# Kernel optimization log

Measured on AMD Instinct MI355X. Metric: run time of the kernel, lower is better.

The kernel has to match this reference:

```python
import jax, jax.numpy as jnp
import numpy as np

B, C, D, H, W = 2, 96, 40, 96, 96
K = 256
OUT = (7, 7, 7)        # (PD, PH, PW)
SCALE = 0.25           # x/y spatial scale
SCALE_D = 0.5          # z (depth) spatial scale
SR = 2                 # sampling_ratio


def setup_inputs() -> dict:
    key = jax.random.key(0)
    k1, k2, k3, k4 = jax.random.split(key, 4)
    x = jax.random.normal(k1, (B, C, D, H, W), dtype=jnp.float32)
    # ROIs in original-image coordinates: x/y in [0, W/SCALE), z in [0, D/SCALE_D)
    img_w, img_h, img_d = W / SCALE, H / SCALE, D / SCALE_D
    bidx = jax.random.randint(k2, (K, 1), 0, B).astype(jnp.float32)
    starts = jax.random.uniform(k3, (K, 3)) * jnp.array([img_w * 0.7, img_h * 0.7, img_d * 0.7])
    sizes = 8.0 + jax.random.uniform(k4, (K, 3)) * jnp.array([img_w * 0.3, img_h * 0.3, img_d * 0.3])
    ends = starts + sizes
    rois = jnp.concatenate([bidx, starts, ends], axis=1).astype(jnp.float32)  # [K,7]
    return {"input_tensor": x, "rois": rois}


def _lin(coord, size):
    # Trilinear 1D component: indices low/high + weights, zeroed outside [-1, size].
    valid = (coord >= -1.0) & (coord <= size)
    c = jnp.clip(coord, 0.0, size - 1)
    low = jnp.floor(c).astype(jnp.int32)
    high = jnp.minimum(low + 1, size - 1)
    frac = c - low.astype(c.dtype)
    wl = jnp.where(valid, 1.0 - frac, 0.0)
    wh = jnp.where(valid, frac, 0.0)
    return low, high, wl, wh


def _sample_coords(start, length, pooled, sr):
    # start, length: [K] -> sample coords [K, pooled*sr]
    bin_sz = length / pooled
    p = jnp.arange(pooled, dtype=start.dtype)
    s = (jnp.arange(sr, dtype=start.dtype) + 0.5) / sr
    c = start[:, None, None] + (p[None, :, None] + s[None, None, :]) * bin_sz[:, None, None]
    return c.reshape(start.shape[0], pooled * sr)


def reference(input_tensor, rois):
    PD, PH, PW = OUT
    bidx = rois[:, 0].astype(jnp.int32)
    x1 = rois[:, 1] * SCALE; y1 = rois[:, 2] * SCALE; z1 = rois[:, 3] * SCALE_D
    x2 = rois[:, 4] * SCALE; y2 = rois[:, 5] * SCALE; z2 = rois[:, 6] * SCALE_D
    rw = jnp.maximum(x2 - x1, 1.0)
    rh = jnp.maximum(y2 - y1, 1.0)
    rd = jnp.maximum(z2 - z1, 1.0)
    cz = _sample_coords(z1, rd, PD, SR)  # [K, PD*SR]
    cy = _sample_coords(y1, rh, PH, SR)  # [K, PH*SR]
    cx = _sample_coords(x1, rw, PW, SR)  # [K, PW*SR]
    zl, zh, wzl, wzh = _lin(cz, D)
    yl, yh, wyl, wyh = _lin(cy, H)
    xl, xh, wxl, wxh = _lin(cx, W)
    b = bidx[:, None, None, None]

    def gather(zi, yi, xi):
        # advanced indexing -> [K, Zs, Ys, Xs, C]
        return input_tensor[b, :, zi[:, :, None, None], yi[:, None, :, None], xi[:, None, None, :]]

    out = jnp.zeros((K, PD * SR, PH * SR, PW * SR, C), dtype=input_tensor.dtype)
    for zi, wz in ((zl, wzl), (zh, wzh)):
        for yi, wy in ((yl, wyl), (yh, wyh)):
            for xi, wx in ((xl, wxl), (xh, wxh)):
                w = wz[:, :, None, None] * wy[:, None, :, None] * wx[:, None, None, :]
                out = out + gather(zi, yi, xi) * w[..., None]
    # average the SR^3 samples inside each output bin
    out = out.reshape(K, PD, SR, PH, SR, PW, SR, C).mean(axis=(2, 4, 6))
    return out.transpose(0, 4, 1, 2, 3)  # [K, C, PD, PH, PW]
```

## Files before the change

### kernel.cpp

```cpp
#include <hip/hip_runtime.h>
#include <hip/hip_fp16.h>


#define Bn 2
#define Cn 96
#define Dn 40
#define Hn 96
#define Wn 96
#define Kn 256
#define CELLS 343
#define NS 14
#define MAXZ 18
#define MAXY 32
#define MAXROWS (MAXZ * MAXY)
#define SLOTS 18
#define DHWc (Dn * Hn * Wn)

typedef float float2u __attribute__((ext_vector_type(2), aligned(4)));

__global__ __launch_bounds__(256) void roialign3d_kernel(
    const float* __restrict__ x,
    const float* __restrict__ rois,
    float* __restrict__ out)
{
    const int k   = blockIdx.x;
    const int c   = blockIdx.y;
    const int tid = threadIdx.x;

    __shared__ __half s_xi[MAXROWS * NS];
    __shared__ int    s_rowoff[MAXROWS];
    __shared__ int    s_lo[2][NS];
    __shared__ int    s_hi[2][NS];
    __shared__ float  s_wl[2][NS];
    __shared__ float  s_wh[2][NS];

    const float rb  = rois[k*7+0];
    const float rx1 = rois[k*7+1]*0.25f, ry1 = rois[k*7+2]*0.25f, rz1 = rois[k*7+3]*0.5f;
    const float rx2 = rois[k*7+4]*0.25f, ry2 = rois[k*7+5]*0.25f, rz2 = rois[k*7+6]*0.5f;
    const int   bidx = (int)rb;
    const float binx = fmaxf(rx2-rx1, 1.0f) / 7.0f;
    const float biny = fmaxf(ry2-ry1, 1.0f) / 7.0f;
    const float binz = fmaxf(rz2-rz1, 1.0f) / 7.0f;

    const int slot = tid / NS;
    const int xs   = tid - slot * NS;
    float wxl, wxh; int xlo;
    {
        const float cx = rx1 + ((float)(xs >> 1) + ((float)(xs & 1) + 0.5f) * 0.5f) * binx;
        const bool valid = (cx >= -1.0f) && (cx <= (float)Wn);
        const float cc = fminf(fmaxf(cx, 0.0f), (float)(Wn - 1));
        int lo = (int)floorf(cc);
        const float frac = cc - (float)lo;
        wxl = valid ? 1.0f - frac : 0.0f;
        wxh = valid ? frac : 0.0f;
        if (lo >= Wn - 1) { wxh = wxl; wxl = 0.0f; lo = Wn - 2; }
        xlo = lo;
    }

    if (tid < 2 * NS) {
        const int axis = tid / NS;
        const int i    = tid - axis * NS;
        const float start = (axis == 0) ? rz1 : ry1;
        const float bin   = (axis == 0) ? binz : biny;
        const float size  = (axis == 0) ? (float)Dn : (float)Hn;
        const float c0 = start + ((float)(i >> 1) + ((float)(i & 1) + 0.5f) * 0.5f) * bin;
        const bool valid = (c0 >= -1.0f) && (c0 <= size);
        const float cc = fminf(fmaxf(c0, 0.0f), size - 1.0f);
        const int lo = (int)floorf(cc);
        const float frac = cc - (float)lo;
        s_lo[axis][i] = lo;
        s_hi[axis][i] = min(lo + 1, (int)size - 1);
        s_wl[axis][i] = valid ? 1.0f - frac : 0.0f;
        s_wh[axis][i] = valid ? frac : 0.0f;
    }
    __syncthreads();

    const int zmin = s_lo[0][0], ymin = s_lo[1][0];
    const int Zd = min(s_hi[0][NS-1] - zmin + 1, MAXZ);
    const int Yd = min(s_hi[1][NS-1] - ymin + 1, MAXY);
    const int nrows = Zd * Yd;

    for (int r = tid; r < nrows; r += 256) {
        const int zd = r / Yd;
        const int yd = r - zd * Yd;
        s_rowoff[r] = ((zmin + zd) * Hn + (ymin + yd)) * Wn;
    }
    __syncthreads();

    const float* xb = x + ((long long)bidx * Cn + c) * DHWc;
    if (slot < SLOTS) {
        int row = slot;
        for (; row + 3 * SLOTS < nrows; row += 4 * SLOTS) {
            const int r0 = row, r1 = row + SLOTS, r2 = row + 2*SLOTS, r3 = row + 3*SLOTS;
            const int o0 = s_rowoff[r0], o1 = s_rowoff[r1],
                      o2 = s_rowoff[r2], o3 = s_rowoff[r3];
            const float2u f0 = *(const float2u*)(xb + o0 + xlo);
            const float2u f1 = *(const float2u*)(xb + o1 + xlo);
            const float2u f2 = *(const float2u*)(xb + o2 + xlo);
            const float2u f3 = *(const float2u*)(xb + o3 + xlo);
            s_xi[r0 * NS + xs] = __float2half(wxl * f0.x + wxh * f0.y);
            s_xi[r1 * NS + xs] = __float2half(wxl * f1.x + wxh * f1.y);
            s_xi[r2 * NS + xs] = __float2half(wxl * f2.x + wxh * f2.y);
            s_xi[r3 * NS + xs] = __float2half(wxl * f3.x + wxh * f3.y);
        }
        for (; row < nrows; row += SLOTS) {
            const float2u f = *(const float2u*)(xb + s_rowoff[row] + xlo);
            s_xi[row * NS + xs] = __float2half(wxl * f.x + wxh * f.y);
        }
    }
    __syncthreads();

    for (int cell = tid; cell < CELLS; cell += 256) {
        const int pw = cell % 7;
        const int ph = (cell / 7) % 7;
        const int pd = cell / 49;
        const int px2 = pw * 2;

        float acc = 0.0f;
        #pragma unroll
        for (int iz = 0; iz < 2; ++iz) {
            const int   zi  = pd * 2 + iz;
            const int   zl  = s_lo[0][zi] - zmin;
            const int   zh  = s_hi[0][zi] - zmin;
            const float wz0 = s_wl[0][zi], wz1 = s_wh[0][zi];
            #pragma unroll
            for (int iy = 0; iy < 2; ++iy) {
                const int   yi  = ph * 2 + iy;
                const int   yl  = s_lo[1][yi] - ymin;
                const int   yh  = s_hi[1][yi] - ymin;
                const float wy0 = s_wl[1][yi], wy1 = s_wh[1][yi];

                const __half2 a00 = *(const __half2*)&s_xi[(zl * Yd + yl) * NS + px2];
                const __half2 a01 = *(const __half2*)&s_xi[(zl * Yd + yh) * NS + px2];
                const __half2 a10 = *(const __half2*)&s_xi[(zh * Yd + yl) * NS + px2];
                const __half2 a11 = *(const __half2*)&s_xi[(zh * Yd + yh) * NS + px2];

                const float sx00 = __low2float(a00) + __high2float(a00);
                const float sx01 = __low2float(a01) + __high2float(a01);
                const float sx10 = __low2float(a10) + __high2float(a10);
                const float sx11 = __low2float(a11) + __high2float(a11);
                acc += wz0 * (wy0 * sx00 + wy1 * sx01)
                     + wz1 * (wy0 * sx10 + wy1 * sx11);
            }
        }
        out[((long long)k * Cn + c) * CELLS + cell] = acc * 0.125f;
    }
}

extern "C" void kernel_launch(void* const* d_in, const int* in_sizes, int n_in,
                              void* d_out, int out_size, void* d_ws, size_t ws_size,
                              hipStream_t stream) {
    const float* x    = (const float*)d_in[0];
    const float* rois = (const float*)d_in[1];
    float* out        = (float*)d_out;

    dim3 grid(Kn, Cn);
    roialign3d_kernel<<<grid, dim3(256), 0, stream>>>(x, rois, out);
}
```

Measured before the change: 108.5 us.

## Process two channels per block with 384 threads and hoisted per-cell indices

Each block now handles two channels in sequence, so the ROI setup, row-offset table and per-cell z/y indices and weights are computed once and reused for both channels. The block grows to 384 threads so that one thread covers each of the 343 output cells and 27 row slots gather the x-interpolated rows. The change trades half as many blocks, and therefore less parallelism, plus an extra barrier per channel, for less repeated setup work.

```diff
diff --git a/kernel.cpp b/kernel.cpp
--- a/kernel.cpp
+++ b/kernel.cpp
@@ -13,18 +13,20 @@
 #define MAXZ 18
 #define MAXY 32
 #define MAXROWS (MAXZ * MAXY)
-#define SLOTS 18
+#define NT 384
+#define SLOTS 27
+#define CPB 2
 #define DHWc (Dn * Hn * Wn)
 
 typedef float float2u __attribute__((ext_vector_type(2), aligned(4)));
 
-__global__ __launch_bounds__(256) void roialign3d_kernel(
+__global__ __launch_bounds__(NT) void roialign3d_kernel(
     const float* __restrict__ x,
     const float* __restrict__ rois,
     float* __restrict__ out)
 {
     const int k   = blockIdx.x;
-    const int c   = blockIdx.y;
+    const int c0  = blockIdx.y * CPB;
     const int tid = threadIdx.x;
 
     __shared__ __half s_xi[MAXROWS * NS];
@@ -63,9 +65,9 @@
         const float start = (axis == 0) ? rz1 : ry1;
         const float bin   = (axis == 0) ? binz : biny;
         const float size  = (axis == 0) ? (float)Dn : (float)Hn;
-        const float c0 = start + ((float)(i >> 1) + ((float)(i & 1) + 0.5f) * 0.5f) * bin;
-        const bool valid = (c0 >= -1.0f) && (c0 <= size);
-        const float cc = fminf(fmaxf(c0, 0.0f), size - 1.0f);
+        const float c0f = start + ((float)(i >> 1) + ((float)(i & 1) + 0.5f) * 0.5f) * bin;
+        const bool valid = (c0f >= -1.0f) && (c0f <= size);
+        const float cc = fminf(fmaxf(c0f, 0.0f), size - 1.0f);
         const int lo = (int)floorf(cc);
         const float frac = cc - (float)lo;
         s_lo[axis][i] = lo;
@@ -80,70 +82,82 @@
     const int Yd = min(s_hi[1][NS-1] - ymin + 1, MAXY);
     const int nrows = Zd * Yd;
 
-    for (int r = tid; r < nrows; r += 256) {
+    for (int r = tid; r < nrows; r += NT) {
         const int zd = r / Yd;
         const int yd = r - zd * Yd;
         s_rowoff[r] = ((zmin + zd) * Hn + (ymin + yd)) * Wn;
     }
     __syncthreads();
 
-    const float* xb = x + ((long long)bidx * Cn + c) * DHWc;
-    if (slot < SLOTS) {
-        int row = slot;
-        for (; row + 3 * SLOTS < nrows; row += 4 * SLOTS) {
-            const int r0 = row, r1 = row + SLOTS, r2 = row + 2*SLOTS, r3 = row + 3*SLOTS;
-            const int o0 = s_rowoff[r0], o1 = s_rowoff[r1],
-                      o2 = s_rowoff[r2], o3 = s_rowoff[r3];
-            const float2u f0 = *(const float2u*)(xb + o0 + xlo);
-            const float2u f1 = *(const float2u*)(xb + o1 + xlo);
-            const float2u f2 = *(const float2u*)(xb + o2 + xlo);
-            const float2u f3 = *(const float2u*)(xb + o3 + xlo);
-            s_xi[r0 * NS + xs] = __float2half(wxl * f0.x + wxh * f0.y);
-            s_xi[r1 * NS + xs] = __float2half(wxl * f1.x + wxh * f1.y);
-            s_xi[r2 * NS + xs] = __float2half(wxl * f2.x + wxh * f2.y);
-            s_xi[r3 * NS + xs] = __float2half(wxl * f3.x + wxh * f3.y);
+    const bool cellact = (tid < CELLS);
+    int   zY[4], yN[4];
+    float wzv[4], wyv[4];
+    if (cellact) {
+        const int pw = tid % 7;
+        const int t7 = tid / 7;
+        const int ph = t7 % 7;
+        const int pd = t7 / 7;
+        const int px2 = pw * 2;
+        #pragma unroll
+        for (int iz = 0; iz < 2; ++iz) {
+            const int zi = pd * 2 + iz;
+            zY[iz*2+0] = (s_lo[0][zi] - zmin) * (Yd * NS);
+            zY[iz*2+1] = (s_hi[0][zi] - zmin) * (Yd * NS);
+            wzv[iz*2+0] = s_wl[0][zi];
+            wzv[iz*2+1] = s_wh[0][zi];
         }
-        for (; row < nrows; row += SLOTS) {
-            const float2u f = *(const float2u*)(xb + s_rowoff[row] + xlo);
-            s_xi[row * NS + xs] = __float2half(wxl * f.x + wxh * f.y);
+        #pragma unroll
+        for (int iy = 0; iy < 2; ++iy) {
+            const int yi = ph * 2 + iy;
+            yN[iy*2+0] = (s_lo[1][yi] - ymin) * NS + px2;
+            yN[iy*2+1] = (s_hi[1][yi] - ymin) * NS + px2;
+            wyv[iy*2+0] = s_wl[1][yi];
+            wyv[iy*2+1] = s_wh[1][yi];
         }
     }
-    __syncthreads();
 
-    for (int cell = tid; cell < CELLS; cell += 256) {
-        const int pw = cell % 7;
-        const int ph = (cell / 7) % 7;
-        const int pd = cell / 49;
-        const int px2 = pw * 2;
+    const float* xb0 = x + ((long long)bidx * Cn + c0) * DHWc;
+    const long long outbase = ((long long)k * Cn + c0) * CELLS;
 
-        float acc = 0.0f;
-        #pragma unroll
-        for (int iz = 0; iz < 2; ++iz) {
-            const int   zi  = pd * 2 + iz;
-            const int   zl  = s_lo[0][zi] - zmin;
-            const int   zh  = s_hi[0][zi] - zmin;
-            const float wz0 = s_wl[0][zi], wz1 = s_wh[0][zi];
-            #pragma unroll
-            for (int iy = 0; iy < 2; ++iy) {
-                const int   yi  = ph * 2 + iy;
-                const int   yl  = s_lo[1][yi] - ymin;
-                const int   yh  = s_hi[1][yi] - ymin;
-                const float wy0 = s_wl[1][yi], wy1 = s_wh[1][yi];
-
-                const __half2 a00 = *(const __half2*)&s_xi[(zl * Yd + yl) * NS + px2];
-                const __half2 a01 = *(const __half2*)&s_xi[(zl * Yd + yh) * NS + px2];
-                const __half2 a10 = *(const __half2*)&s_xi[(zh * Yd + yl) * NS + px2];
-                const __half2 a11 = *(const __half2*)&s_xi[(zh * Yd + yh) * NS + px2];
-
-                const float sx00 = __low2float(a00) + __high2float(a00);
-                const float sx01 = __low2float(a01) + __high2float(a01);
-                const float sx10 = __low2float(a10) + __high2float(a10);
-                const float sx11 = __low2float(a11) + __high2float(a11);
-                acc += wz0 * (wy0 * sx00 + wy1 * sx01)
-                     + wz1 * (wy0 * sx10 + wy1 * sx11);
+    for (int cc = 0; cc < CPB; ++cc) {
+        const float* xb = xb0 + (long long)cc * DHWc;
+        if (slot < SLOTS) {
+            int row = slot;
+            for (; row + 3 * SLOTS < nrows; row += 4 * SLOTS) {
+                const int r0 = row, r1 = row + SLOTS, r2 = row + 2*SLOTS, r3 = row + 3*SLOTS;
+                const int o0 = s_rowoff[r0], o1 = s_rowoff[r1],
+                          o2 = s_rowoff[r2], o3 = s_rowoff[r3];
+                const float2u f0 = *(const float2u*)(xb + o0 + xlo);
+                const float2u f1 = *(const float2u*)(xb + o1 + xlo);
+                const float2u f2 = *(const float2u*)(xb + o2 + xlo);
+                const float2u f3 = *(const float2u*)(xb + o3 + xlo);
+                s_xi[r0 * NS + xs] = __float2half(wxl * f0.x + wxh * f0.y);
+                s_xi[r1 * NS + xs] = __float2half(wxl * f1.x + wxh * f1.y);
+                s_xi[r2 * NS + xs] = __float2half(wxl * f2.x + wxh * f2.y);
+                s_xi[r3 * NS + xs] = __float2half(wxl * f3.x + wxh * f3.y);
+            }
+            for (; row < nrows; row += SLOTS) {
+                const float2u f = *(const float2u*)(xb + s_rowoff[row] + xlo);
+                s_xi[row * NS + xs] = __float2half(wxl * f.x + wxh * f.y);
             }
         }
-        out[((long long)k * Cn + c) * CELLS + cell] = acc * 0.125f;
+        __syncthreads();
+
+        if (cellact) {
+            float acc = 0.0f;
+            #pragma unroll
+            for (int b = 0; b < 4; ++b) {
+                float accb = 0.0f;
+                #pragma unroll
+                for (int a = 0; a < 4; ++a) {
+                    const __half2 h = *(const __half2*)&s_xi[zY[a] + yN[b]];
+                    accb += wzv[a] * (__low2float(h) + __high2float(h));
+                }
+                acc += wyv[b] * accb;
+            }
+            out[outbase + (long long)cc * CELLS + tid] = acc * 0.125f;
+        }
+        __syncthreads();
     }
 }
 
@@ -154,6 +168,6 @@
     const float* rois = (const float*)d_in[1];
     float* out        = (float*)d_out;
 
-    dim3 grid(Kn, Cn);
-    roialign3d_kernel<<<grid, dim3(256), 0, stream>>>(x, rois, out);
+    dim3 grid(Kn, Cn / CPB);
+    roialign3d_kernel<<<grid, dim3(NT), 0, stream>>>(x, rois, out);
 }
```

Measured after the change: 111.6 us. +2.9%, slower.
